# Optimization experiments

Hardware: AMD Instinct MI355X
Metric: run time of the kernel (lower is better)

## Reference

```python
import jax, jax.numpy as jnp
import numpy as np

G = 256          # children of root (groups)
C = 256          # children per group (leaves per group)
D = G + G * C    # total softmax slots: root range [0,G), group g range [G+g*C, G+(g+1)*C)


def setup_inputs() -> dict:
    key = jax.random.key(0)
    k1, k2 = jax.random.split(key)
    B = 4096
    batch_predictions = jax.random.normal(k1, (B, D), dtype=jnp.float32)
    targets = jax.random.randint(k2, (B,), 0, G * C, dtype=jnp.int64)
    return {"batch_predictions": batch_predictions, "targets": targets}


def reference(batch_predictions, targets):
    # targets are leaf ids in [0, G*C); decompose into (group, index_in_parent)
    B = batch_predictions.shape[0]
    group = targets // C          # index_in_parent at root level
    child = targets % C           # index_in_parent at group level
    rows = jnp.arange(B)

    # Root-level cross entropy over slots [0, G)
    root_logp = jax.nn.log_softmax(batch_predictions[:, :G], axis=-1)  # [B, G]
    root_ce = -root_logp[rows, group]

    # Group-level cross entropy over slots [G + g*C, G + (g+1)*C), gathered per sample
    col_idx = G + group[:, None] * C + jnp.arange(C)[None, :]          # [B, C]
    group_logits = jnp.take_along_axis(batch_predictions, col_idx, axis=1)
    group_logp = jax.nn.log_softmax(group_logits, axis=-1)             # [B, C]
    group_ce = -group_logp[rows, child]

    # alpha = 1.0 at every internal node; sum over path, mean over batch
    return jnp.mean(root_ce + group_ce)
```

## Files before the change

kernel.cpp:

```cpp
#include <hip/hip_runtime.h>
#include <hip/hip_bf16.h>


#define HSM_G 256
#define HSM_C 256
#define HSM_D (HSM_G + HSM_G * HSM_C)
#define HSM_B 4096

__global__ __launch_bounds__(256) void hsm_loss_kernel(
    const float* __restrict__ pred,
    const int*   __restrict__ tgt,
    float* __restrict__ out)
{
    const int row = blockIdx.x;
    const int tid = threadIdx.x;
    const int t     = tgt[row];
    const int group = t >> 8;
    const int child = t & 255;

    const float* rowp = pred + (size_t)row * HSM_D;

    __shared__ float sred[4];
    __shared__ float sx[2];

    float ce_sum = 0.0f;

#pragma unroll
    for (int phase = 0; phase < 2; ++phase) {
        const int base = (phase == 0) ? 0 : (HSM_G + group * HSM_C);
        const int idx  = (phase == 0) ? group : child;

        const float x = rowp[base + tid];
        if (tid == idx) sx[phase] = x;

        float m = x;
        for (int off = 32; off > 0; off >>= 1)
            m = fmaxf(m, __shfl_down(m, off));
        if ((tid & 63) == 0) sred[tid >> 6] = m;
        __syncthreads();
        m = fmaxf(fmaxf(sred[0], sred[1]), fmaxf(sred[2], sred[3]));
        __syncthreads();

        float s = expf(x - m);
        for (int off = 32; off > 0; off >>= 1)
            s += __shfl_down(s, off);
        if ((tid & 63) == 0) sred[tid >> 6] = s;
        __syncthreads();
        s = sred[0] + sred[1] + sred[2] + sred[3];
        __syncthreads();

        ce_sum += -(sx[phase] - m - logf(s));
    }

    if (tid == 0)
        atomicAdd(out, ce_sum * (1.0f / (float)HSM_B));
}

extern "C" void kernel_launch(void* const* d_in, const int* in_sizes, int n_in,
                              void* d_out, int out_size, void* d_ws, size_t ws_size,
                              hipStream_t stream) {
    const float* pred = (const float*)d_in[0];
    const int*   tgt  = (const int*)d_in[1];
    float* out = (float*)d_out;

    hipMemsetAsync(out, 0, sizeof(float), stream);

    hsm_loss_kernel<<<HSM_B, 256, 0, stream>>>(pred, tgt, out);
}
```

Before: 1.170 ms.

## Map one wavefront per row with float4 loads and two-stage deterministic reduction

```diff
diff --git a/kernel.cpp b/kernel.cpp
--- a/kernel.cpp
+++ b/kernel.cpp
@@ -6,54 +6,70 @@
 #define HSM_C 256
 #define HSM_D (HSM_G + HSM_G * HSM_C)
 #define HSM_B 4096
+#define ROWS_PER_BLOCK 4
+#define N_BLOCKS (HSM_B / ROWS_PER_BLOCK)
 
-__global__ __launch_bounds__(256) void hsm_loss_kernel(
+__global__ __launch_bounds__(256) void hsm_partial_kernel(
     const float* __restrict__ pred,
     const int*   __restrict__ tgt,
-    float* __restrict__ out)
+    float*       __restrict__ partial)
 {
-    const int row = blockIdx.x;
-    const int tid = threadIdx.x;
+    const int wave = threadIdx.x >> 6;
+    const int lane = threadIdx.x & 63;
+    const int row  = blockIdx.x * ROWS_PER_BLOCK + wave;
+
     const int t     = tgt[row];
     const int group = t >> 8;
     const int child = t & 255;
-
     const float* rowp = pred + (size_t)row * HSM_D;
 
-    __shared__ float sred[4];
-    __shared__ float sx[2];
-
-    float ce_sum = 0.0f;
+    float ce = 0.0f;
 
 #pragma unroll
     for (int phase = 0; phase < 2; ++phase) {
-        const int base = (phase == 0) ? 0 : (HSM_G + group * HSM_C);
+        const int base = (phase == 0) ? 0 : (HSM_G + (group << 8));
         const int idx  = (phase == 0) ? group : child;
 
-        const float x = rowp[base + tid];
-        if (tid == idx) sx[phase] = x;
+        const float4 v = *(const float4*)(rowp + base + (lane << 2));
 
-        float m = x;
-        for (int off = 32; off > 0; off >>= 1)
-            m = fmaxf(m, __shfl_down(m, off));
-        if ((tid & 63) == 0) sred[tid >> 6] = m;
-        __syncthreads();
-        m = fmaxf(fmaxf(sred[0], sred[1]), fmaxf(sred[2], sred[3]));
-        __syncthreads();
+        const int comp = idx & 3;
+        const float cand = (comp == 0) ? v.x : (comp == 1) ? v.y
+                         : (comp == 2) ? v.z : v.w;
+        const float xt = __shfl(cand, idx >> 2);
 
-        float s = expf(x - m);
-        for (int off = 32; off > 0; off >>= 1)
-            s += __shfl_down(s, off);
-        if ((tid & 63) == 0) sred[tid >> 6] = s;
-        __syncthreads();
-        s = sred[0] + sred[1] + sred[2] + sred[3];
-        __syncthreads();
+        float m = fmaxf(fmaxf(v.x, v.y), fmaxf(v.z, v.w));
+#pragma unroll
+        for (int off = 32; off; off >>= 1) m = fmaxf(m, __shfl_xor(m, off));
 
-        ce_sum += -(sx[phase] - m - logf(s));
+        float s = expf(v.x - m) + expf(v.y - m) + expf(v.z - m) + expf(v.w - m);
+#pragma unroll
+        for (int off = 32; off; off >>= 1) s += __shfl_xor(s, off);
+
+        ce += (m + logf(s)) - xt;
     }
 
+    __shared__ float sred[ROWS_PER_BLOCK];
+    if (lane == 0) sred[wave] = ce;
+    __syncthreads();
+    if (threadIdx.x == 0)
+        partial[blockIdx.x] = sred[0] + sred[1] + sred[2] + sred[3];
+}
+
+__global__ __launch_bounds__(256) void hsm_final_kernel(
+    const float* __restrict__ partial,
+    float*       __restrict__ out)
+{
+    const int tid = threadIdx.x;
+    const float4 v = ((const float4*)partial)[tid];
+    float s = v.x + v.y + v.z + v.w;
+#pragma unroll
+    for (int off = 32; off; off >>= 1) s += __shfl_xor(s, off);
+
+    __shared__ float sred[4];
+    if ((tid & 63) == 0) sred[tid >> 6] = s;
+    __syncthreads();
     if (tid == 0)
-        atomicAdd(out, ce_sum * (1.0f / (float)HSM_B));
+        out[0] = (sred[0] + sred[1] + sred[2] + sred[3]) * (1.0f / (float)HSM_B);
 }
 
 extern "C" void kernel_launch(void* const* d_in, const int* in_sizes, int n_in,
@@ -61,9 +77,9 @@
                               hipStream_t stream) {
     const float* pred = (const float*)d_in[0];
     const int*   tgt  = (const int*)d_in[1];
-    float* out = (float*)d_out;
+    float* out     = (float*)d_out;
+    float* partial = (float*)d_ws;
 
-    hipMemsetAsync(out, 0, sizeof(float), stream);
-
-    hsm_loss_kernel<<<HSM_B, 256, 0, stream>>>(pred, tgt, out);
+    hsm_partial_kernel<<<N_BLOCKS, 256, 0, stream>>>(pred, tgt, partial);
+    hsm_final_kernel<<<1, 256, 0, stream>>>(partial, out);
 }
```

Result: faster. 1.113 ms (-4.9%).
